# Optimization experiments

Hardware: AMD Instinct MI355X
Metric: run time of the kernel (lower is better)

The kernel has to match this reference:

```python
import jax, jax.numpy as jnp
import numpy as np

NUM_LAYERS = 8
HIDDEN = 128
BATCH = 262144
SKIP_CONNECTION = True
BIAS_ENABLED = True


def setup_inputs() -> dict:
    key = jax.random.key(0)
    kx, kw, kb = jax.random.split(key, 3)
    x = jax.random.normal(kx, (BATCH, HIDDEN), dtype=jnp.float32)
    # scale weights ~ 1/sqrt(fan_in) so activations stay O(1) across 8 layers
    w = jax.random.normal(kw, (NUM_LAYERS, HIDDEN, HIDDEN), dtype=jnp.float32) * (1.0 / np.sqrt(HIDDEN))
    b = jax.random.normal(kb, (NUM_LAYERS, HIDDEN), dtype=jnp.float32) * 0.01
    return {"x": x, "w": w, "b": b}


def reference(x, w, b):
    # Fused elastic MLP, full-width (active_neurons == hidden for every layer).
    # Per the Triton forward kernel: every layer (including the last) applies
    # ReLU, and with skip_connection the input block is added AFTER the
    # activation for layers > 0.
    h = x
    for layer in range(NUM_LAYERS):
        h = jax.nn.relu(jnp.einsum('bi,ji->bj', h, w[layer]) + (b[layer] if BIAS_ENABLED else 0.0))
        if SKIP_CONNECTION and layer > 0:
            h = h + x  # input_dim == hidden, skip-add over full width
    return h
```

## Files before the change

### kernel.cpp

```cpp
#include <hip/hip_runtime.h>
#include <hip/hip_bf16.h>


typedef __bf16 bf16_t;
typedef __bf16 bf16x8 __attribute__((ext_vector_type(8)));
typedef __bf16 bf16x4 __attribute__((ext_vector_type(4)));
typedef float floatx4 __attribute__((ext_vector_type(4)));

#define HID 128
#define NLAYERS 8
#define TM 128
#define LDH 136

__global__ __launch_bounds__(256) void wconv_kernel(const float* __restrict__ w,
                                                    bf16_t* __restrict__ wb) {
    int i = (blockIdx.x * 256 + threadIdx.x) * 4;
    floatx4 v = *(const floatx4*)&w[i];
    bf16x4 o = { (bf16_t)v[0], (bf16_t)v[1], (bf16_t)v[2], (bf16_t)v[3] };
    *(bf16x4*)&wb[i] = o;
}

__global__ __launch_bounds__(256, 2) void mlp_kernel(
    const float* __restrict__ x, const bf16_t* __restrict__ wb,
    const float* __restrict__ bias, float* __restrict__ out)
{
    __shared__ __align__(16) bf16_t hs[TM][LDH];
    __shared__ __align__(16) bf16_t wsh[HID][LDH];

    const int tid  = threadIdx.x;
    const int wave = tid >> 6;
    const int lane = tid & 63;
    const int c16  = lane & 15;
    const int quad = lane >> 4;
    const int m0 = (wave >> 1) * 64;
    const int n0 = (wave & 1) * 64;
    const long rowbase = (long)blockIdx.x * TM;
    const int jb = m0 + quad * 4;

    floatx4 xr[4][4];
#pragma unroll
    for (int ni = 0; ni < 4; ++ni) {
        const float* xrow = x + (rowbase + n0 + ni*16 + c16) * HID;
#pragma unroll
        for (int mi = 0; mi < 4; ++mi)
            xr[mi][ni] = *(const floatx4*)&xrow[jb + mi*16];
    }
#pragma unroll
    for (int ni = 0; ni < 4; ++ni) {
        bf16_t* hrow = &hs[n0 + ni*16 + c16][0];
#pragma unroll
        for (int mi = 0; mi < 4; ++mi) {
            floatx4 v = xr[mi][ni];
            bf16x4 o = { (bf16_t)v[0], (bf16_t)v[1], (bf16_t)v[2], (bf16_t)v[3] };
            *(bf16x4*)&hrow[jb + mi*16] = o;
        }
    }

    const bf16x8* wbv = (const bf16x8*)wb;
    bf16x8 wreg[8];
#pragma unroll
    for (int p = 0; p < 8; ++p) wreg[p] = wbv[p*256 + tid];
    floatx4 bnext[4];
#pragma unroll
    for (int mi = 0; mi < 4; ++mi) bnext[mi] = *(const floatx4*)&bias[jb + mi*16];

    for (int l = 0; l < NLAYERS; ++l) {
#pragma unroll
        for (int p = 0; p < 8; ++p) {
            int f = p*256 + tid;
            *(bf16x8*)&wsh[f >> 4][(f & 15) * 8] = wreg[p];
        }
        __syncthreads();

        floatx4 acc[4][4];
#pragma unroll
        for (int mi = 0; mi < 4; ++mi)
#pragma unroll
          for (int ni = 0; ni < 4; ++ni)
            acc[mi][ni] = bnext[mi];

        if (l + 1 < NLAYERS) {
#pragma unroll
            for (int p = 0; p < 8; ++p) wreg[p] = wbv[(l+1)*2048 + p*256 + tid];
#pragma unroll
            for (int mi = 0; mi < 4; ++mi)
                bnext[mi] = *(const floatx4*)&bias[(l+1)*HID + jb + mi*16];
        }

#pragma unroll
        for (int k = 0; k < 4; ++k) {
            const int kc = k*32 + quad*8;
            bf16x8 af[4], bf[4];
#pragma unroll
            for (int mi = 0; mi < 4; ++mi)
                af[mi] = *(const bf16x8*)&wsh[m0 + mi*16 + c16][kc];
#pragma unroll
            for (int ni = 0; ni < 4; ++ni)
                bf[ni] = *(const bf16x8*)&hs[n0 + ni*16 + c16][kc];
#pragma unroll
            for (int mi = 0; mi < 4; ++mi)
#pragma unroll
              for (int ni = 0; ni < 4; ++ni)
                acc[mi][ni] = __builtin_amdgcn_mfma_f32_16x16x32_bf16(
                                  af[mi], bf[ni], acc[mi][ni], 0, 0, 0);
        }
        __syncthreads();

        if (l < NLAYERS - 1) {
#pragma unroll
            for (int ni = 0; ni < 4; ++ni) {
                bf16_t* hrow = &hs[n0 + ni*16 + c16][0];
#pragma unroll
                for (int mi = 0; mi < 4; ++mi) {
                    floatx4 v = acc[mi][ni];
                    float s0 = fmaxf(v[0], 0.0f), s1 = fmaxf(v[1], 0.0f);
                    float s2 = fmaxf(v[2], 0.0f), s3 = fmaxf(v[3], 0.0f);
                    if (l > 0) {
                        floatx4 xv = xr[mi][ni];
                        s0 += xv[0]; s1 += xv[1]; s2 += xv[2]; s3 += xv[3];
                    }
                    bf16x4 o = { (bf16_t)s0, (bf16_t)s1, (bf16_t)s2, (bf16_t)s3 };
                    *(bf16x4*)&hrow[jb + mi*16] = o;
                }
            }
        } else {
#pragma unroll
            for (int ni = 0; ni < 4; ++ni) {
                float* orow = out + (rowbase + n0 + ni*16 + c16) * HID;
#pragma unroll
                for (int mi = 0; mi < 4; ++mi) {
                    floatx4 v = acc[mi][ni];
                    floatx4 xv = xr[mi][ni];
                    floatx4 o;
                    o[0] = fmaxf(v[0], 0.0f) + xv[0];
                    o[1] = fmaxf(v[1], 0.0f) + xv[1];
                    o[2] = fmaxf(v[2], 0.0f) + xv[2];
                    o[3] = fmaxf(v[3], 0.0f) + xv[3];
                    *(floatx4*)&orow[jb + mi*16] = o;
                }
            }
        }
    }
}

extern "C" void kernel_launch(void* const* d_in, const int* in_sizes, int n_in,
                              void* d_out, int out_size, void* d_ws, size_t ws_size,
                              hipStream_t stream) {
    const float* x = (const float*)d_in[0];
    const float* w = (const float*)d_in[1];
    const float* b = (const float*)d_in[2];
    float* out = (float*)d_out;
    bf16_t* wb = (bf16_t*)d_ws;

    wconv_kernel<<<NLAYERS*HID*HID/(256*4), 256, 0, stream>>>(w, wb);

    const int nblocks = 262144 / TM;
    mlp_kernel<<<nblocks, 256, 0, stream>>>(x, wb, b, out);
}
```

Baseline: 288.7 us.

## Keep activations in registers via 32x32 MFMA and double-buffer swizzled weights

Each wave now owns 32 rows and computes the full 128 outputs with 32x32x16 MFMAs. Activations stay in registers between layers, and cross-lane shuffles turn the accumulator layout into the next layer's B fragment, so the shared-memory activation tile and its stores and loads go away. Weights are double-buffered in an XOR-swizzled shared layout to avoid bank conflicts, which cuts to one barrier per layer, and bias is pre-converted to bf16. The cost is more register pressure and shuffle traffic, plus an extra bf16 rounding of the bias.

```diff
diff --git a/kernel.cpp b/kernel.cpp
--- a/kernel.cpp
+++ b/kernel.cpp
@@ -3,142 +3,171 @@
 
 
 typedef __bf16 bf16_t;
+typedef __bf16 bf16x4 __attribute__((ext_vector_type(4)));
 typedef __bf16 bf16x8 __attribute__((ext_vector_type(8)));
-typedef __bf16 bf16x4 __attribute__((ext_vector_type(4)));
 typedef float floatx4 __attribute__((ext_vector_type(4)));
+typedef float floatx16 __attribute__((ext_vector_type(16)));
+typedef unsigned int uint2v __attribute__((ext_vector_type(2)));
+typedef unsigned int uint4v __attribute__((ext_vector_type(4)));
 
 #define HID 128
-#define NLAYERS 8
-#define TM 128
-#define LDH 136
+#define NL 8
 
 __global__ __launch_bounds__(256) void wconv_kernel(const float* __restrict__ w,
-                                                    bf16_t* __restrict__ wb) {
-    int i = (blockIdx.x * 256 + threadIdx.x) * 4;
-    floatx4 v = *(const floatx4*)&w[i];
-    bf16x4 o = { (bf16_t)v[0], (bf16_t)v[1], (bf16_t)v[2], (bf16_t)v[3] };
-    *(bf16x4*)&wb[i] = o;
+                                                    const float* __restrict__ b,
+                                                    bf16_t* __restrict__ wb,
+                                                    bf16_t* __restrict__ bb) {
+    if (blockIdx.x < 128) {
+        int i = (blockIdx.x * 256 + threadIdx.x) * 4;
+        floatx4 v = *(const floatx4*)&w[i];
+        bf16x4 o = { (bf16_t)v[0], (bf16_t)v[1], (bf16_t)v[2], (bf16_t)v[3] };
+        *(bf16x4*)&wb[i] = o;
+    } else {
+        int i = threadIdx.x * 4;
+        floatx4 v = *(const floatx4*)&b[i];
+        bf16x4 o = { (bf16_t)v[0], (bf16_t)v[1], (bf16_t)v[2], (bf16_t)v[3] };
+        *(bf16x4*)&bb[i] = o;
+    }
+}
+
+__device__ __forceinline__ void build_bfrag(const floatx16 hv[4], int H, bf16x8 bfr[8]) {
+#pragma unroll
+    for (int t = 0; t < 4; ++t)
+#pragma unroll
+        for (int q = 0; q < 2; ++q) {
+            bf16x4 plo = { (bf16_t)hv[t][8*q+0], (bf16_t)hv[t][8*q+1],
+                           (bf16_t)hv[t][8*q+2], (bf16_t)hv[t][8*q+3] };
+            bf16x4 phi = { (bf16_t)hv[t][8*q+4], (bf16_t)hv[t][8*q+5],
+                           (bf16_t)hv[t][8*q+6], (bf16_t)hv[t][8*q+7] };
+            uint2v ulo = __builtin_bit_cast(uint2v, plo);
+            uint2v uhi = __builtin_bit_cast(uint2v, phi);
+            unsigned sx = H ? ulo[0] : uhi[0];
+            unsigned sy = H ? ulo[1] : uhi[1];
+            unsigned rx = (unsigned)__shfl_xor((int)sx, 32, 64);
+            unsigned ry = (unsigned)__shfl_xor((int)sy, 32, 64);
+            uint4v u;
+            u[0] = H ? rx : ulo[0];
+            u[1] = H ? ry : ulo[1];
+            u[2] = H ? uhi[0] : rx;
+            u[3] = H ? uhi[1] : ry;
+            bfr[2*t + q] = __builtin_bit_cast(bf16x8, u);
+        }
 }
 
 __global__ __launch_bounds__(256, 2) void mlp_kernel(
     const float* __restrict__ x, const bf16_t* __restrict__ wb,
-    const float* __restrict__ bias, float* __restrict__ out)
+    const bf16_t* __restrict__ bb, float* __restrict__ out)
 {
-    __shared__ __align__(16) bf16_t hs[TM][LDH];
-    __shared__ __align__(16) bf16_t wsh[HID][LDH];
+    __shared__ __align__(16) bf16_t wsh[2][HID * HID];
 
     const int tid  = threadIdx.x;
     const int wave = tid >> 6;
     const int lane = tid & 63;
-    const int c16  = lane & 15;
-    const int quad = lane >> 4;
-    const int m0 = (wave >> 1) * 64;
-    const int n0 = (wave & 1) * 64;
-    const long rowbase = (long)blockIdx.x * TM;
-    const int jb = m0 + quad * 4;
+    const int H = lane >> 5;
+    const int c = lane & 31;
+    const long gb = ((long)blockIdx.x * 4 + wave) * 32;
+    const float* xrow = x + (gb + c) * HID;
 
     floatx4 xr[4][4];
 #pragma unroll
-    for (int ni = 0; ni < 4; ++ni) {
-        const float* xrow = x + (rowbase + n0 + ni*16 + c16) * HID;
+    for (int mi = 0; mi < 4; ++mi)
 #pragma unroll
-        for (int mi = 0; mi < 4; ++mi)
-            xr[mi][ni] = *(const floatx4*)&xrow[jb + mi*16];
-    }
+        for (int g = 0; g < 4; ++g)
+            xr[mi][g] = *(const floatx4*)&xrow[32*mi + 8*g + 4*H];
+
+    const bf16x8* wbv = (const bf16x8*)wb;
+    bf16x8 wstg[8];
 #pragma unroll
-    for (int ni = 0; ni < 4; ++ni) {
-        bf16_t* hrow = &hs[n0 + ni*16 + c16][0];
+    for (int p = 0; p < 8; ++p) wstg[p] = wbv[p*256 + tid];
+
+    bf16x8 bfr[8];
+    {
+        floatx16 hv[4];
 #pragma unroll
-        for (int mi = 0; mi < 4; ++mi) {
-            floatx4 v = xr[mi][ni];
-            bf16x4 o = { (bf16_t)v[0], (bf16_t)v[1], (bf16_t)v[2], (bf16_t)v[3] };
-            *(bf16x4*)&hrow[jb + mi*16] = o;
-        }
+        for (int t = 0; t < 4; ++t)
+#pragma unroll
+            for (int r = 0; r < 16; ++r)
+                hv[t][r] = xr[t][r >> 2][r & 3];
+        build_bfrag(hv, H, bfr);
     }
 
-    const bf16x8* wbv = (const bf16x8*)wb;
-    bf16x8 wreg[8];
 #pragma unroll
-    for (int p = 0; p < 8; ++p) wreg[p] = wbv[p*256 + tid];
-    floatx4 bnext[4];
-#pragma unroll
-    for (int mi = 0; mi < 4; ++mi) bnext[mi] = *(const floatx4*)&bias[jb + mi*16];
+    for (int p = 0; p < 8; ++p) {
+        int f = p*256 + tid;
+        int m = f >> 4, t = f & 15;
+        *(bf16x8*)&wsh[0][m*HID + ((t ^ (m & 7)) * 8)] = wstg[p];
+    }
+    __syncthreads();
 
-    for (int l = 0; l < NLAYERS; ++l) {
-#pragma unroll
-        for (int p = 0; p < 8; ++p) {
-            int f = p*256 + tid;
-            *(bf16x8*)&wsh[f >> 4][(f & 15) * 8] = wreg[p];
-        }
-        __syncthreads();
-
-        floatx4 acc[4][4];
+    for (int l = 0; l < NL; ++l) {
+        floatx16 acc[4];
 #pragma unroll
         for (int mi = 0; mi < 4; ++mi)
 #pragma unroll
-          for (int ni = 0; ni < 4; ++ni)
-            acc[mi][ni] = bnext[mi];
+            for (int g = 0; g < 4; ++g) {
+                bf16x4 bv = *(const bf16x4*)&bb[l*HID + 32*mi + 8*g + 4*H];
+#pragma unroll
+                for (int k = 0; k < 4; ++k) acc[mi][4*g + k] = (float)bv[k];
+            }
 
-        if (l + 1 < NLAYERS) {
+        if (l + 1 < NL) {
 #pragma unroll
-            for (int p = 0; p < 8; ++p) wreg[p] = wbv[(l+1)*2048 + p*256 + tid];
+            for (int p = 0; p < 8; ++p) wstg[p] = wbv[(l+1)*2048 + p*256 + tid];
+        }
+
+        const bf16_t* wbuf = wsh[l & 1];
+        bf16x8 wf[2][4];
+#pragma unroll
+        for (int mi = 0; mi < 4; ++mi)
+            wf[0][mi] = *(const bf16x8*)&wbuf[(32*mi + c)*HID + ((H ^ (c & 7)) * 8)];
+#pragma unroll
+        for (int s = 0; s < 8; ++s) {
+            if (s + 1 < 8) {
+                const int tc = 2*(s+1) + H;
+#pragma unroll
+                for (int mi = 0; mi < 4; ++mi)
+                    wf[(s+1) & 1][mi] =
+                        *(const bf16x8*)&wbuf[(32*mi + c)*HID + ((tc ^ (c & 7)) * 8)];
+            }
 #pragma unroll
             for (int mi = 0; mi < 4; ++mi)
-                bnext[mi] = *(const floatx4*)&bias[(l+1)*HID + jb + mi*16];
+                acc[mi] = __builtin_amdgcn_mfma_f32_32x32x16_bf16(
+                              wf[s & 1][mi], bfr[s], acc[mi], 0, 0, 0);
         }
 
+        if (l + 1 < NL) {
 #pragma unroll
-        for (int k = 0; k < 4; ++k) {
-            const int kc = k*32 + quad*8;
-            bf16x8 af[4], bf[4];
-#pragma unroll
-            for (int mi = 0; mi < 4; ++mi)
-                af[mi] = *(const bf16x8*)&wsh[m0 + mi*16 + c16][kc];
-#pragma unroll
-            for (int ni = 0; ni < 4; ++ni)
-                bf[ni] = *(const bf16x8*)&hs[n0 + ni*16 + c16][kc];
+            for (int p = 0; p < 8; ++p) {
+                int f = p*256 + tid;
+                int m = f >> 4, t = f & 15;
+                *(bf16x8*)&wsh[(l+1) & 1][m*HID + ((t ^ (m & 7)) * 8)] = wstg[p];
+            }
+        }
+
+        if (l < NL - 1) {
+            floatx16 hv[4];
 #pragma unroll
             for (int mi = 0; mi < 4; ++mi)
 #pragma unroll
-              for (int ni = 0; ni < 4; ++ni)
-                acc[mi][ni] = __builtin_amdgcn_mfma_f32_16x16x32_bf16(
-                                  af[mi], bf[ni], acc[mi][ni], 0, 0, 0);
-        }
-        __syncthreads();
-
-        if (l < NLAYERS - 1) {
+                for (int r = 0; r < 16; ++r) {
+                    float v = fmaxf(acc[mi][r], 0.0f);
+                    if (l > 0) v += xr[mi][r >> 2][r & 3];
+                    hv[mi][r] = v;
+                }
+            build_bfrag(hv, H, bfr);
+            __syncthreads();
+        } else {
+            float* orow = out + (gb + c) * HID;
 #pragma unroll
-            for (int ni = 0; ni < 4; ++ni) {
-                bf16_t* hrow = &hs[n0 + ni*16 + c16][0];
+            for (int mi = 0; mi < 4; ++mi)
 #pragma unroll
-                for (int mi = 0; mi < 4; ++mi) {
-                    floatx4 v = acc[mi][ni];
-                    float s0 = fmaxf(v[0], 0.0f), s1 = fmaxf(v[1], 0.0f);
-                    float s2 = fmaxf(v[2], 0.0f), s3 = fmaxf(v[3], 0.0f);
-                    if (l > 0) {
-                        floatx4 xv = xr[mi][ni];
-                        s0 += xv[0]; s1 += xv[1]; s2 += xv[2]; s3 += xv[3];
-                    }
-                    bf16x4 o = { (bf16_t)s0, (bf16_t)s1, (bf16_t)s2, (bf16_t)s3 };
-                    *(bf16x4*)&hrow[jb + mi*16] = o;
+                for (int g = 0; g < 4; ++g) {
+                    floatx4 o;
+#pragma unroll
+                    for (int k = 0; k < 4; ++k)
+                        o[k] = fmaxf(acc[mi][4*g + k], 0.0f) + xr[mi][g][k];
+                    *(floatx4*)&orow[32*mi + 8*g + 4*H] = o;
                 }
-            }
-        } else {
-#pragma unroll
-            for (int ni = 0; ni < 4; ++ni) {
-                float* orow = out + (rowbase + n0 + ni*16 + c16) * HID;
-#pragma unroll
-                for (int mi = 0; mi < 4; ++mi) {
-                    floatx4 v = acc[mi][ni];
-                    floatx4 xv = xr[mi][ni];
-                    floatx4 o;
-                    o[0] = fmaxf(v[0], 0.0f) + xv[0];
-                    o[1] = fmaxf(v[1], 0.0f) + xv[1];
-                    o[2] = fmaxf(v[2], 0.0f) + xv[2];
-                    o[3] = fmaxf(v[3], 0.0f) + xv[3];
-                    *(floatx4*)&orow[jb + mi*16] = o;
-                }
-            }
         }
     }
 }
@@ -151,9 +180,10 @@
     const float* b = (const float*)d_in[2];
     float* out = (float*)d_out;
     bf16_t* wb = (bf16_t*)d_ws;
+    bf16_t* bbb = (bf16_t*)d_ws + 131072;
 
-    wconv_kernel<<<NLAYERS*HID*HID/(256*4), 256, 0, stream>>>(w, wb);
+    wconv_kernel<<<129, 256, 0, stream>>>(w, b, wb, bbb);
 
-    const int nblocks = 262144 / TM;
-    mlp_kernel<<<nblocks, 256, 0, stream>>>(x, wb, b, out);
+    const int nblocks = 262144 / 128;
+    mlp_kernel<<<nblocks, 256, 0, stream>>>(x, wb, bbb, out);
 }
```

Result: slower. 328.3 us (+13.7%).
